# Kernel tuning notes

Measured on AMD Instinct MI355X. Metric: run time of the kernel, lower is better.

Reference implementation:

```python
import jax, jax.numpy as jnp
import numpy as np
from jax.scipy.ndimage import map_coordinates

IMG = 256
N_ANG = 50
BATCH = 4
N_CNN = 32
IN_CH = 2


def _circle_mask(S):
    c = (S - 1) / 2.0
    yy, xx = jnp.meshgrid(jnp.arange(S, dtype=jnp.float32), jnp.arange(S, dtype=jnp.float32), indexing='ij')
    return (((yy - c) ** 2 + (xx - c) ** 2) <= (S / 2.0) ** 2).astype(jnp.float32)


def radon_forward(img, angles):
    # img [B,1,S,S] -> sinogram [B,1,A,S]; parallel-beam, clip_to_circle=True
    S = img.shape[-1]
    c = (S - 1) / 2.0
    img = img * _circle_mask(S)
    t = jnp.arange(S, dtype=jnp.float32) - c        # integration coord
    s = jnp.arange(S, dtype=jnp.float32) - c        # detector coord
    cos = jnp.cos(angles)[:, None, None]
    sin = jnp.sin(angles)[:, None, None]
    x = s[None, None, :] * cos - t[None, :, None] * sin   # [A,S,S]
    y = s[None, None, :] * sin + t[None, :, None] * cos
    coords = jnp.stack([y + c, x + c])                    # [2,A,S,S] (row, col)
    samp = jax.vmap(lambda im: map_coordinates(im, coords, order=1, mode='constant', cval=0.0))(img[:, 0])  # [B,A,S,S]
    return samp.sum(axis=2)[:, None]                      # sum over ray param -> [B,1,A,S]


def filter_sinogram(sino):
    # Ram-Lak FFT filter with zero-padding + FBP normalization
    S = sino.shape[-1]
    A = sino.shape[2]
    P = max(64, int(2 ** np.ceil(np.log2(2 * S))))
    f = jnp.fft.rfft(jnp.pad(sino, ((0, 0), (0, 0), (0, 0), (0, P - S))), axis=-1)
    ramp = 2.0 * jnp.fft.rfftfreq(P).astype(jnp.float32)
    out = jnp.fft.irfft(f * ramp, n=P, axis=-1)[..., :S]
    return out * (np.pi / (2.0 * A))


def radon_backprojection(sino, angles):
    # sino [B,1,A,S] -> image [B,1,S,S]
    B, _, A, S = sino.shape
    c = (S - 1) / 2.0
    yy, xx = jnp.meshgrid(jnp.arange(S, dtype=jnp.float32) - c, jnp.arange(S, dtype=jnp.float32) - c, indexing='ij')
    cos = jnp.cos(angles)[:, None, None]
    sin = jnp.sin(angles)[:, None, None]
    det = xx[None] * cos + yy[None] * sin + c             # [A,S,S] detector coord
    sino2 = sino[:, 0]                                    # [B,A,S]

    def interp_one(sino_a, idx):
        # sino_a [B,S], idx [S,S] -> [B,S,S] linear interp, zero outside
        i0 = jnp.clip(jnp.floor(idx).astype(jnp.int32), 0, S - 2)
        w = idx - i0
        v = sino_a[:, i0] * (1.0 - w) + sino_a[:, i0 + 1] * w
        valid = (idx >= 0.0) & (idx <= S - 1.0)
        return jnp.where(valid, v, 0.0)

    bp = jax.vmap(interp_one, in_axes=(1, 0))(sino2, det).sum(axis=0)  # [B,S,S]
    return (bp * _circle_mask(S))[:, None]


def conv2d(x, w, b):
    y = jax.lax.conv_general_dilated(x, w, (1, 1), 'SAME', dimension_numbers=('NCHW', 'OIHW', 'NCHW'))
    return y + b[None, :, None, None]


def setup_inputs() -> dict:
    key = jax.random.key(0)
    ks = jax.random.split(key, 10)
    angles = jnp.asarray(np.linspace(0, np.pi, N_ANG, endpoint=False), dtype=jnp.float32)
    return {
        'x_sinogram': jax.random.normal(ks[0], (BATCH, 1, N_ANG, IMG), dtype=jnp.float32),
        'y_img_prev': jax.random.normal(ks[1], (BATCH, 1, IMG, IMG), dtype=jnp.float32),
        'y_img_concat_prev': jax.random.normal(ks[2], (BATCH, 1, IMG, IMG), dtype=jnp.float32),
        'angles': angles,
        'step': jnp.float32(1.0),
        'w1': jax.random.normal(ks[3], (N_CNN, IN_CH, 3, 3), dtype=jnp.float32) * 0.1,
        'b1': jnp.zeros((N_CNN,), dtype=jnp.float32),
        'w2': jax.random.normal(ks[4], (N_CNN, N_CNN, 3, 3), dtype=jnp.float32) * 0.1,
        'b2': jnp.zeros((N_CNN,), dtype=jnp.float32),
        'w3': jax.random.normal(ks[5], (1, N_CNN, 3, 3), dtype=jnp.float32) * 0.1,
        'b3': jnp.zeros((1,), dtype=jnp.float32),
    }


def reference(x_sinogram, y_img_prev, y_img_concat_prev, angles, step, w1, b1, w2, b2, w3, b3):
    Ay = radon_forward(y_img_prev, angles)                 # [B,1,A,S]
    diff = Ay - x_sinogram
    filt = filter_sinogram(diff)
    fbp = radon_backprojection(filt, angles)               # [B,1,S,S]
    y_img_update = y_img_prev + step * fbp
    y_cat = jnp.concatenate([y_img_update, y_img_concat_prev], axis=1)  # [B,2,S,S]
    h = jax.nn.relu(conv2d(y_cat, w1, b1))
    h = jax.nn.relu(conv2d(h, w2, b2))
    y_img = conv2d(h, w3, b3)
    return (y_img, y_img_update)
```

## Files before the change

### kernel.cpp

```cpp
#include <hip/hip_runtime.h>
#include <math.h>

#define IMGS 256
#define NANG 50
#define BATCH 4
#define NCNN 32
#define PIX (IMGS*IMGS)
#define NPIX (BATCH*PIX)

#define PROW 258
#define PPIX (PROW*PROW)
#define PB   (PPIX*NCNN)

#define OFF_FILT  0
#define OFF_W2BF  51200
#define OFF_H1P   55808

static constexpr double PI_D = 3.14159265358979323846;

typedef unsigned short u16;
typedef unsigned int   u32;
typedef unsigned long long u64;
typedef __bf16 bfrag __attribute__((ext_vector_type(8)));
typedef float  ffrag __attribute__((ext_vector_type(4)));

__device__ __forceinline__ u16 f2bf(float f) {
    u32 u = __float_as_uint(f);
    u += 0x7fffu + ((u >> 16) & 1u);
    return (u16)(u >> 16);
}

#define RPITCH_D 131
__global__ __launch_bounds__(1024, 4) void k_A(const float* __restrict__ angles,
                                               const float* __restrict__ yprev,
                                               const float* __restrict__ xsino,
                                               const float* __restrict__ w2,
                                               float* __restrict__ ws) {
    __shared__ u16 limg[258 * 262];
    __shared__ float spart[1024];
    __shared__ float staps[512];
    __shared__ float srow[256];
    int tid = threadIdx.x;
    int gid = blockIdx.x;
    if (gid >= 200) {
        int i = (gid - 200) * 1024 + tid;
        if (i < 9216) {
            int t = i >> 10, oc = (i >> 5) & 31, ic = i & 31;
            ((u16*)(ws + OFF_W2BF))[i] = f2bf(w2[(oc * 32 + ic) * 9 + t]);
        }
        return;
    }
    u32* l32 = (u32*)limg;
    int ra = gid;
    int a = ra % NANG, b = ra / NANG;

    if (tid < 511) {
        int d = tid - 255;
        int n = d < 0 ? -d : d;
        double g;
        if (n == 0) {
            g = 0.5;
        } else {
            double th = PI_D * (double)n / 256.0;
            double S = (256.0 * cos(255.0 * th) - 255.0 * cos(256.0 * th) - 1.0)
                       / (2.0 * (1.0 - cos(th)));
            double sign = (n & 1) ? -1.0 : 1.0;
            g = (sign + S / 128.0) / 512.0;
        }
        staps[tid] = (float)(g * PI_D / 100.0);
    }

    for (int z = tid; z < 772; z += 1024) {
        int addr;
        if (z < 258)      addr = z * RPITCH_D;
        else if (z < 516) addr = (z - 258) * RPITCH_D + 129;
        else if (z < 644) addr = (z - 516) + 1;
        else              addr = 257 * RPITCH_D + (z - 644) + 1;
        l32[addr] = 0;
    }
    const float* __restrict__ src = yprev + b * PIX;
    for (int idx = tid; idx < 16384; idx += 1024) {
        int r = idx >> 6, c4 = (idx & 63) << 2;
        float4 v = *(const float4*)(src + r * 256 + c4);
        float di = (float)r - 127.5f;
        float rr = di * di;
        float d0 = (float)c4 - 127.5f;
        v.x = (rr + d0 * d0 <= 16384.0f) ? v.x : 0.0f;
        v.y = (rr + (d0 + 1.0f) * (d0 + 1.0f) <= 16384.0f) ? v.y : 0.0f;
        v.z = (rr + (d0 + 2.0f) * (d0 + 2.0f) <= 16384.0f) ? v.z : 0.0f;
        v.w = (rr + (d0 + 3.0f) * (d0 + 3.0f) <= 16384.0f) ? v.w : 0.0f;
        u32 p0 = (u32)f2bf(v.x) | ((u32)f2bf(v.y) << 16);
        u32 p1 = (u32)f2bf(v.z) | ((u32)f2bf(v.w) << 16);
        int dw = (r + 1) * RPITCH_D + (c4 >> 1) + 1;
        l32[dw] = p0; l32[dw + 1] = p1;
    }
    __syncthreads();

    float a_ = angles[a];
    float cs = cosf(a_), sn = sinf(a_);
    int lane = tid & 63, w = tid >> 6;
    int s8 = lane & 7, t8 = lane >> 3;
    int sA = w * 16 + s8;
    float scA = (float)sA - 127.5f;

    float loA = (float)(w * 16) - 127.5f, hiA = loA + 7.0f;
    float loB = loA + 8.0f,               hiB = hiA + 8.0f;
    float s2minA = fminf(loA * loA, hiA * hiA);
    float s2maxA = fmaxf(loA * loA, hiA * hiA);
    float s2minB = fminf(loB * loB, hiB * hiB);
    float s2maxB = fmaxf(loB * loB, hiB * hiB);
    float s2min  = fminf(s2minA, s2minB);
    float s2max  = fmaxf(s2maxA, s2maxB);
    float hmax = sqrtf(16770.25f - s2min);
    int j_lo = max(0, (int)ceilf((120.5f - hmax) * 0.125f));
    int j_hi = min(31, (int)floorf((127.5f + hmax) * 0.125f));

    float tc0 = (float)t8 - 127.5f + 8.0f * (float)j_lo;
    float rowA = scA * sn + tc0 * cs + 127.5f;
    float colA = scA * cs - tc0 * sn + 127.5f;
    float rowB = rowA + 8.0f * sn;
    float colB = colA + 8.0f * cs;
    float cs8 = 8.0f * cs, sn8 = 8.0f * sn;
    float accA = 0.0f, accB = 0.0f;
    #pragma unroll 2
    for (int j = j_lo; j <= j_hi; ++j) {
        float t0j = 8.0f * (float)j - 127.5f;
        float t7j = t0j + 7.0f;
        float tmax2 = fmaxf(t0j * t0j, t7j * t7j);
        if (s2max + tmax2 <= 16384.0f) {
            #pragma unroll
            for (int hh = 0; hh < 2; ++hh) {
                float rowv = hh ? rowB : rowA;
                float colv = hh ? colB : colA;
                float fr = floorf(rowv), fc = floorf(colv);
                float wr = rowv - fr, wc = colv - fc;
                int i0 = (int)fr, j0 = (int)fc;
                int ca = j0 + 2;
                int ka = ca >> 1;
                int sh = (ca & 1) << 4;
                int dw = (i0 + 1) * RPITCH_D + ka;
                u32 A = l32[dw],            C = l32[dw + 1];
                u32 B = l32[dw + RPITCH_D], D = l32[dw + RPITCH_D + 1];
                u32 top = (u32)((((u64)C << 32) | (u64)A) >> sh);
                u32 bot = (u32)((((u64)D << 32) | (u64)B) >> sh);
                float tl = __uint_as_float(top << 16);
                float tr_ = __uint_as_float(top & 0xffff0000u);
                float bl = __uint_as_float(bot << 16);
                float br = __uint_as_float(bot & 0xffff0000u);
                float tv = tl + (tr_ - tl) * wc;
                float bv = bl + (br - bl) * wc;
                float sv = tv + (bv - tv) * wr;
                if (hh) accB += sv; else accA += sv;
            }
        } else {
            #pragma unroll
            for (int hh = 0; hh < 2; ++hh) {
                float rowv = hh ? rowB : rowA;
                float colv = hh ? colB : colA;
                float fr = floorf(rowv), fc = floorf(colv);
                float wr = rowv - fr, wc = colv - fc;
                int i0 = (int)fr, j0 = (int)fc;
                bool valid = (rowv > -1.0f) & (rowv < 256.0f) & (colv > -1.0f) & (colv < 256.0f);
                int i0c = min(max(i0, -1), 255);
                int j0c = min(max(j0, -1), 255);
                int ca = j0c + 2;
                int ka = ca >> 1;
                int sh = (ca & 1) << 4;
                int dw = (i0c + 1) * RPITCH_D + ka;
                u32 A = l32[dw],            C = l32[dw + 1];
                u32 B = l32[dw + RPITCH_D], D = l32[dw + RPITCH_D + 1];
                u32 top = (u32)((((u64)C << 32) | (u64)A) >> sh);
                u32 bot = (u32)((((u64)D << 32) | (u64)B) >> sh);
                float tl = __uint_as_float(top << 16);
                float tr_ = __uint_as_float(top & 0xffff0000u);
                float bl = __uint_as_float(bot << 16);
                float br = __uint_as_float(bot & 0xffff0000u);
                float tv = tl + (tr_ - tl) * wc;
                float bv = bl + (br - bl) * wc;
                float sv = tv + (bv - tv) * wr;
                sv = valid ? sv : 0.0f;
                if (hh) accB += sv; else accA += sv;
            }
        }
        rowA += cs8; colA -= sn8; rowB += cs8; colB -= sn8;
    }
    accA += __shfl_xor(accA, 8, 64);
    accA += __shfl_xor(accA, 16, 64);
    accA += __shfl_xor(accA, 32, 64);
    accB += __shfl_xor(accB, 8, 64);
    accB += __shfl_xor(accB, 16, 64);
    accB += __shfl_xor(accB, 32, 64);
    if (t8 == 0) { spart[sA] = accA; spart[sA + 8] = accB; }
    __syncthreads();
    if (tid < 256)
        srow[tid] = spart[tid] - xsino[ra * 256 + tid];
    __syncthreads();
    {
        int s = tid & 255, q = tid >> 8;
        float fa = 0.0f;
        int m0 = q * 64;
        #pragma unroll 8
        for (int m = m0; m < m0 + 64; ++m) fa += srow[m] * staps[s - m + 255];
        spart[tid] = fa;
    }
    __syncthreads();
    if (tid < 256)
        ws[OFF_FILT + ra * 256 + tid] =
            spart[tid] + spart[tid + 256] + spart[tid + 512] + spart[tid + 768];
}

__global__ __launch_bounds__(512, 4) void k_B(const float* __restrict__ angles,
                                              const float* __restrict__ yprev,
                                              const float* __restrict__ yconc,
                                              const float* __restrict__ stepp,
                                              const float* __restrict__ w1,
                                              const float* __restrict__ b1,
                                              float* __restrict__ ws,
                                              float* __restrict__ dout) {
    __shared__ float sf[NANG * 256];
    __shared__ __align__(16) float supd[4][260];
    __shared__ __align__(16) float sy2[4][260];
    __shared__ float scs[NANG], ssn[NANG];
    int tid = threadIdx.x;
    int b = blockIdx.x >> 7, tile = blockIdx.x & 127;
    int y0 = tile << 1;

    {
        const float4* s4 = (const float4*)(ws + OFF_FILT + b * (NANG * 256));
        float4* d4 = (float4*)sf;
        for (int idx = tid; idx < NANG * 64; idx += 512) d4[idx] = s4[idx];
    }
    if (tid < NANG) {
        float a_ = angles[tid];
        scs[tid] = cosf(a_); ssn[tid] = sinf(a_);
    }
    if (tid < 8) supd[tid >> 1][(tid & 1) * 257] = 0.0f;
    for (int idx = tid; idx < 4 * 258; idx += 512) {
        int r = idx / 258, x = idx % 258;
        int iy = y0 - 1 + r, ix = x - 1;
        sy2[r][x] = ((unsigned)iy < 256u && (unsigned)ix < 256u)
                        ? yconc[b * PIX + iy * 256 + ix] : 0.0f;
    }
    if (tid < 144) {
        int px_i = tile * 9 + (tid >> 4), dw = tid & 15;
        if (px_i < 1028) {
            int y, x;
            if (px_i < 516) { y = (px_i < 258) ? 0 : 257; x = px_i % 258; }
            else            { int j = px_i - 516; y = 1 + (j >> 1); x = (j & 1) * 257; }
            u32* p = (u32*)((u16*)(ws + OFF_H1P) + b * PB + (y * PROW + x) * NCNN);
            p[dw] = 0;
        }
    }
    __syncthreads();

    float step = stepp[0];
    {
        int j = tid & 255, r0 = tid >> 8;
        float xx = (float)j - 127.5f;
        float yy0 = (float)(y0 - 1 + r0) - 127.5f;
        float acc[2] = {0.0f, 0.0f};
        #pragma unroll 5
        for (int a = 0; a < NANG; ++a) {
            float cs = scs[a], sn = ssn[a];
            float f0 = xx * cs + yy0 * sn + 127.5f;
            float idxf[2] = {f0, f0 + sn + sn};
            #pragma unroll
            for (int k = 0; k < 2; ++k) {
                float fl = floorf(idxf[k]);
                int i0 = (int)fl;
                i0 = min(max(i0, 0), 254);
                float w = idxf[k] - (float)i0;
                float v = sf[a * 256 + i0] * (1.0f - w) + sf[a * 256 + i0 + 1] * w;
                acc[k] += (idxf[k] >= 0.0f && idxf[k] <= 255.0f) ? v : 0.0f;
            }
        }
        #pragma unroll
        for (int k = 0; k < 2; ++k) {
            int r = r0 + 2 * k;
            int iy = y0 - 1 + r;
            float val = 0.0f;
            if ((unsigned)iy < 256u) {
                float yy = (float)iy - 127.5f;
                float m = (xx * xx + yy * yy <= 16384.0f) ? 1.0f : 0.0f;
                val = yprev[b * PIX + iy * 256 + j] + step * acc[k] * m;
                if (r >= 1 && r <= 2)
                    dout[NPIX + b * PIX + iy * 256 + j] = val;
            }
            supd[r][j + 1] = val;
        }
    }
    __syncthreads();

    {
        int wave = tid >> 6, lane = tid & 63;
        int oc0 = wave * 4;
        float W[72];
        const float4* wsrc = (const float4*)(w1 + oc0 * 18);
        #pragma unroll
        for (int i = 0; i < 18; ++i) ((float4*)W)[i] = wsrc[i];
        float bb0 = b1[oc0], bb1 = b1[oc0 + 1], bb2 = b1[oc0 + 2], bb3 = b1[oc0 + 3];
        u16* h1base = (u16*)(ws + OFF_H1P) + b * PB;
        #pragma unroll
        for (int it = 0; it < 4; ++it) {
            int px0 = it * 128 + lane * 2;
            int rr = px0 >> 8, x0 = px0 & 255;
            int oy = y0 + rr;
            float a00 = bb0, a01 = bb1, a02 = bb2, a03 = bb3;
            float a10 = bb0, a11 = bb1, a12 = bb2, a13 = bb3;
            #pragma unroll
            for (int ky = 0; ky < 3; ++ky) {
                float2 ua = *(const float2*)&supd[rr + ky][x0];
                float2 ub = *(const float2*)&supd[rr + ky][x0 + 2];
                float2 ca = *(const float2*)&sy2[rr + ky][x0];
                float2 cb = *(const float2*)&sy2[rr + ky][x0 + 2];
                float u[4]  = {ua.x, ua.y, ub.x, ub.y};
                float c6[4] = {ca.x, ca.y, cb.x, cb.y};
                #pragma unroll
                for (int kx = 0; kx < 3; ++kx) {
                    int t = ky * 3 + kx;
                    float u0 = u[kx],     c0 = c6[kx];
                    float u1 = u[kx + 1], c1 = c6[kx + 1];
                    a00 += u0 * W[t]      + c0 * W[9 + t];
                    a01 += u0 * W[18 + t] + c0 * W[27 + t];
                    a02 += u0 * W[36 + t] + c0 * W[45 + t];
                    a03 += u0 * W[54 + t] + c0 * W[63 + t];
                    a10 += u1 * W[t]      + c1 * W[9 + t];
                    a11 += u1 * W[18 + t] + c1 * W[27 + t];
                    a12 += u1 * W[36 + t] + c1 * W[45 + t];
                    a13 += u1 * W[54 + t] + c1 * W[63 + t];
                }
            }
            u32 q00 = (u32)f2bf(fmaxf(a00, 0.0f)) | ((u32)f2bf(fmaxf(a01, 0.0f)) << 16);
            u32 q01 = (u32)f2bf(fmaxf(a02, 0.0f)) | ((u32)f2bf(fmaxf(a03, 0.0f)) << 16);
            u32 q10 = (u32)f2bf(fmaxf(a10, 0.0f)) | ((u32)f2bf(fmaxf(a11, 0.0f)) << 16);
            u32 q11 = (u32)f2bf(fmaxf(a12, 0.0f)) | ((u32)f2bf(fmaxf(a13, 0.0f)) << 16);
            u32* op0 = (u32*)(h1base + ((oy + 1) * PROW + (x0 + 1)) * NCNN + oc0);
            u32* op1 = (u32*)(h1base + ((oy + 1) * PROW + (x0 + 2)) * NCNN + oc0);
            op0[0] = q00; op0[1] = q01;
            op1[0] = q10; op1[1] = q11;
        }
    }
}

#define H2PITCH 36
__global__ __launch_bounds__(512, 4) void k_C(const float* __restrict__ b2,
                                              const float* __restrict__ w3,
                                              const float* __restrict__ b3,
                                              float* __restrict__ ws,
                                              float* __restrict__ dout) {
    __shared__ __align__(16) u16 sh2[4 * 258 * H2PITCH];
    __shared__ __align__(8) u32 swp[9 * 16];
    u32* l32 = (u32*)sh2;
    int tid = threadIdx.x;
    int b = blockIdx.x >> 7, tile = blockIdx.x & 127;
    int y0 = tile << 1;

    if (tid < 144) {
        int t = tid >> 4, kd = tid & 15;
        swp[tid] = (u32)f2bf(w3[(2 * kd) * 9 + t]) | ((u32)f2bf(w3[(2 * kd + 1) * 9 + t]) << 16);
    }
    if (tid < 144) {
        int r = tid / 36, rem = tid % 36;
        int col = (rem < 18) ? 0 : 257, dw = rem % 18;
        l32[(r * 258 + col) * 18 + dw] = 0;
    }
    #pragma unroll
    for (int r = 0; r < 4; ++r) {
        int hy = y0 - 1 + r;
        if (hy < 0 || hy > 255)
            for (int idx = tid; idx < 258 * 18; idx += 512)
                l32[r * 258 * 18 + idx] = 0;
    }
    __syncthreads();

    const u16* __restrict__ w2bf = (const u16*)(ws + OFF_W2BF);
    const u16* __restrict__ h1b  = (const u16*)(ws + OFF_H1P) + b * PB;
    int wave = tid >> 6, lane = tid & 63;
    int m = lane & 15, quad = lane >> 4;
    bfrag Bf[9][2];
    #pragma unroll
    for (int t = 0; t < 9; ++t) {
        const u16* wp = w2bf + t * 1024 + m * 32 + quad * 8;
        Bf[t][0] = *(const bfrag*)(wp);
        Bf[t][1] = *(const bfrag*)(wp + 16 * 32);
    }
    float bias0 = b2[m], bias1 = b2[m + 16];
    #pragma unroll
    for (int k = 0; k < 8; ++k) {
        int tl = wave + (k << 3);
        int ridx = tl >> 4, xt = tl & 15;
        int hy = y0 - 1 + ridx;
        bool valid = (unsigned)hy < 256u;
        int hyc = min(max(hy, 0), 255);
        int xs = xt << 4;
        bfrag A0[3], A1[3];
        #pragma unroll
        for (int tx = 0; tx < 3; ++tx)
            A0[tx] = *(const bfrag*)(h1b + ((hyc + 0) * PROW + xs + m + tx) * NCNN + quad * 8);
        #pragma unroll
        for (int tx = 0; tx < 3; ++tx)
            A1[tx] = *(const bfrag*)(h1b + ((hyc + 1) * PROW + xs + m + tx) * NCNN + quad * 8);
        ffrag c0 = {0.f, 0.f, 0.f, 0.f}, c1 = {0.f, 0.f, 0.f, 0.f};
        #pragma unroll
        for (int tx = 0; tx < 3; ++tx) {
            c0 = __builtin_amdgcn_mfma_f32_16x16x32_bf16(A0[tx], Bf[tx][0], c0, 0, 0, 0);
            c1 = __builtin_amdgcn_mfma_f32_16x16x32_bf16(A0[tx], Bf[tx][1], c1, 0, 0, 0);
        }
        #pragma unroll
        for (int tx = 0; tx < 3; ++tx)
            A0[tx] = *(const bfrag*)(h1b + ((hyc + 2) * PROW + xs + m + tx) * NCNN + quad * 8);
        #pragma unroll
        for (int tx = 0; tx < 3; ++tx) {
            c0 = __builtin_amdgcn_mfma_f32_16x16x32_bf16(A1[tx], Bf[3 + tx][0], c0, 0, 0, 0);
            c1 = __builtin_amdgcn_mfma_f32_16x16x32_bf16(A1[tx], Bf[3 + tx][1], c1, 0, 0, 0);
        }
        #pragma unroll
        for (int tx = 0; tx < 3; ++tx) {
            c0 = __builtin_amdgcn_mfma_f32_16x16x32_bf16(A0[tx], Bf[6 + tx][0], c0, 0, 0, 0);
            c1 = __builtin_amdgcn_mfma_f32_16x16x32_bf16(A0[tx], Bf[6 + tx][1], c1, 0, 0, 0);
        }
        if (valid) {
            #pragma unroll
            for (int r = 0; r < 4; ++r) {
                int px = xs + quad * 4 + r;
                u16* op = sh2 + (ridx * 258 + px + 1) * H2PITCH;
                op[m]      = f2bf(fmaxf(c0[r] + bias0, 0.0f));
                op[m + 16] = f2bf(fmaxf(c1[r] + bias1, 0.0f));
            }
        }
    }
    __syncthreads();

    {
        int rr = tid >> 8, x = tid & 255;
        int oy = y0 + rr;
        float acc = b3[0];
        #pragma unroll
        for (int ky = 0; ky < 3; ++ky) {
            #pragma unroll
            for (int cx = 0; cx < 3; ++cx) {
                int t = ky * 3 + cx;
                const uint2* q2 = (const uint2*)(l32 + ((rr + ky) * 258 + x + cx) * 18);
                const uint2* w2p = (const uint2*)(swp + t * 16);
                #pragma unroll
                for (int kd = 0; kd < 8; ++kd) {
                    uint2 hv = q2[kd];
                    uint2 wv = w2p[kd];
                    acc += __uint_as_float(hv.x << 16) * __uint_as_float(wv.x << 16)
                         + __uint_as_float(hv.x & 0xffff0000u) * __uint_as_float(wv.x & 0xffff0000u)
                         + __uint_as_float(hv.y << 16) * __uint_as_float(wv.y << 16)
                         + __uint_as_float(hv.y & 0xffff0000u) * __uint_as_float(wv.y & 0xffff0000u);
                }
            }
        }
        dout[b * PIX + oy * 256 + x] = acc;
    }
}

extern "C" void kernel_launch(void* const* d_in, const int* in_sizes, int n_in,
                              void* d_out, int out_size, void* d_ws, size_t ws_size,
                              hipStream_t stream) {
    const float* xsino  = (const float*)d_in[0];
    const float* yprev  = (const float*)d_in[1];
    const float* yconc  = (const float*)d_in[2];
    const float* angles = (const float*)d_in[3];
    const float* stepp  = (const float*)d_in[4];
    const float* w1 = (const float*)d_in[5];
    const float* b1 = (const float*)d_in[6];
    const float* w2 = (const float*)d_in[7];
    const float* b2 = (const float*)d_in[8];
    const float* w3 = (const float*)d_in[9];
    const float* b3 = (const float*)d_in[10];
    float* out = (float*)d_out;
    float* ws  = (float*)d_ws;

    k_A<<<209, 1024, 0, stream>>>(angles, yprev, xsino, w2, ws);
    k_B<<<BATCH * 128, 512, 0, stream>>>(angles, yprev, yconc, stepp, w1, b1, ws, out);
    k_C<<<BATCH * 128, 512, 0, stream>>>(b2, w3, b3, ws, out);
}
```

Before: 172.4 us.

## Store conv1 output in channel-planar layout and read filtered sinogram from global

Changes the intermediate h1 buffer from pixel-interleaved 32-channel layout to 8 planes of 4 channels each, so each wave in k_B writes contiguous 8-byte chunks per pixel. k_C reassembles MFMA A-fragments from two planes with two 8-byte loads each. k_B also drops its 51 KB shared-memory copy of the filtered sinogram and gathers directly from global/L1, and raises the launch-bounds occupancy hint from 4 to 6. The risks are more scattered global gathers in the backprojection and split, narrower loads in k_C.

Measured after the change: 233.7 us. 35.5% more time.

```diff
diff --git a/kernel.cpp b/kernel.cpp
--- a/kernel.cpp
+++ b/kernel.cpp
@@ -209,7 +209,7 @@
             spart[tid] + spart[tid + 256] + spart[tid + 512] + spart[tid + 768];
 }
 
-__global__ __launch_bounds__(512, 4) void k_B(const float* __restrict__ angles,
+__global__ __launch_bounds__(512, 6) void k_B(const float* __restrict__ angles,
                                               const float* __restrict__ yprev,
                                               const float* __restrict__ yconc,
                                               const float* __restrict__ stepp,
@@ -217,19 +217,14 @@
                                               const float* __restrict__ b1,
                                               float* __restrict__ ws,
                                               float* __restrict__ dout) {
-    __shared__ float sf[NANG * 256];
     __shared__ __align__(16) float supd[4][260];
     __shared__ __align__(16) float sy2[4][260];
     __shared__ float scs[NANG], ssn[NANG];
     int tid = threadIdx.x;
     int b = blockIdx.x >> 7, tile = blockIdx.x & 127;
     int y0 = tile << 1;
-
-    {
-        const float4* s4 = (const float4*)(ws + OFF_FILT + b * (NANG * 256));
-        float4* d4 = (float4*)sf;
-        for (int idx = tid; idx < NANG * 64; idx += 512) d4[idx] = s4[idx];
-    }
+    const float* __restrict__ sfg = ws + OFF_FILT + b * (NANG * 256);
+
     if (tid < NANG) {
         float a_ = angles[tid];
         scs[tid] = cosf(a_); ssn[tid] = sinf(a_);
@@ -242,12 +237,13 @@
                         ? yconc[b * PIX + iy * 256 + ix] : 0.0f;
     }
     if (tid < 144) {
-        int px_i = tile * 9 + (tid >> 4), dw = tid & 15;
+        int px_i = tile * 9 + (tid >> 4);
         if (px_i < 1028) {
             int y, x;
             if (px_i < 516) { y = (px_i < 258) ? 0 : 257; x = px_i % 258; }
             else            { int j = px_i - 516; y = 1 + (j >> 1); x = (j & 1) * 257; }
-            u32* p = (u32*)((u16*)(ws + OFF_H1P) + b * PB + (y * PROW + x) * NCNN);
+            int plane = (tid >> 1) & 7, dw = tid & 1;
+            u32* p = (u32*)((u16*)(ws + OFF_H1P) + b * PB + (plane * PPIX + y * PROW + x) * 4);
             p[dw] = 0;
         }
     }
@@ -270,7 +266,7 @@
                 int i0 = (int)fl;
                 i0 = min(max(i0, 0), 254);
                 float w = idxf[k] - (float)i0;
-                float v = sf[a * 256 + i0] * (1.0f - w) + sf[a * 256 + i0 + 1] * w;
+                float v = sfg[a * 256 + i0] * (1.0f - w) + sfg[a * 256 + i0 + 1] * w;
                 acc[k] += (idxf[k] >= 0.0f && idxf[k] <= 255.0f) ? v : 0.0f;
             }
         }
@@ -299,7 +295,7 @@
         #pragma unroll
         for (int i = 0; i < 18; ++i) ((float4*)W)[i] = wsrc[i];
         float bb0 = b1[oc0], bb1 = b1[oc0 + 1], bb2 = b1[oc0 + 2], bb3 = b1[oc0 + 3];
-        u16* h1base = (u16*)(ws + OFF_H1P) + b * PB;
+        u16* pl = (u16*)(ws + OFF_H1P) + b * PB + wave * (PPIX * 4);
         #pragma unroll
         for (int it = 0; it < 4; ++it) {
             int px0 = it * 128 + lane * 2;
@@ -334,15 +330,24 @@
             u32 q01 = (u32)f2bf(fmaxf(a02, 0.0f)) | ((u32)f2bf(fmaxf(a03, 0.0f)) << 16);
             u32 q10 = (u32)f2bf(fmaxf(a10, 0.0f)) | ((u32)f2bf(fmaxf(a11, 0.0f)) << 16);
             u32 q11 = (u32)f2bf(fmaxf(a12, 0.0f)) | ((u32)f2bf(fmaxf(a13, 0.0f)) << 16);
-            u32* op0 = (u32*)(h1base + ((oy + 1) * PROW + (x0 + 1)) * NCNN + oc0);
-            u32* op1 = (u32*)(h1base + ((oy + 1) * PROW + (x0 + 2)) * NCNN + oc0);
-            op0[0] = q00; op0[1] = q01;
-            op1[0] = q10; op1[1] = q11;
+            u32* op = (u32*)(pl + ((oy + 1) * PROW + (x0 + 1)) * 4);
+            *(uint2*)(op)     = make_uint2(q00, q01);
+            *(uint2*)(op + 2) = make_uint2(q10, q11);
         }
     }
 }
 
 #define H2PITCH 36
+__device__ __forceinline__ bfrag ld_frag(const u16* __restrict__ h1b, int q,
+                                         int row, int col) {
+    const u16* base = h1b + (row * PROW + col) * 4;
+    uint2 lo = *(const uint2*)(base + (2 * q)     * (PPIX * 4));
+    uint2 hi = *(const uint2*)(base + (2 * q + 1) * (PPIX * 4));
+    bfrag A;
+    ((uint2*)&A)[0] = lo;
+    ((uint2*)&A)[1] = hi;
+    return A;
+}
 __global__ __launch_bounds__(512, 4) void k_C(const float* __restrict__ b2,
                                               const float* __restrict__ w3,
                                               const float* __restrict__ b3,
@@ -396,10 +401,10 @@
         bfrag A0[3], A1[3];
         #pragma unroll
         for (int tx = 0; tx < 3; ++tx)
-            A0[tx] = *(const bfrag*)(h1b + ((hyc + 0) * PROW + xs + m + tx) * NCNN + quad * 8);
+            A0[tx] = ld_frag(h1b, quad, hyc + 0, xs + m + tx);
         #pragma unroll
         for (int tx = 0; tx < 3; ++tx)
-            A1[tx] = *(const bfrag*)(h1b + ((hyc + 1) * PROW + xs + m + tx) * NCNN + quad * 8);
+            A1[tx] = ld_frag(h1b, quad, hyc + 1, xs + m + tx);
         ffrag c0 = {0.f, 0.f, 0.f, 0.f}, c1 = {0.f, 0.f, 0.f, 0.f};
         #pragma unroll
         for (int tx = 0; tx < 3; ++tx) {
@@ -408,7 +413,7 @@
         }
         #pragma unroll
         for (int tx = 0; tx < 3; ++tx)
-            A0[tx] = *(const bfrag*)(h1b + ((hyc + 2) * PROW + xs + m + tx) * NCNN + quad * 8);
+            A0[tx] = ld_frag(h1b, quad, hyc + 2, xs + m + tx);
         #pragma unroll
         for (int tx = 0; tx < 3; ++tx) {
             c0 = __builtin_amdgcn_mfma_f32_16x16x32_bf16(A1[tx], Bf[3 + tx][0], c0, 0, 0, 0);
```

## Fuse backprojection, conv1 and conv2/conv3 into one kernel with LDS-resident h1

Applied to the files above, without the earlier changes.

Merges k_B and k_C into a single kernel that recomputes an 8-row halo of the updated image per tile, runs conv1 into shared memory in two column halves, then runs the MFMA conv2 and conv3 straight from LDS. This removes the global round trip of the 32-channel bf16 h1 tensor and one kernel launch. In exchange it recomputes backprojection and conv1 on halo rows (8 rows computed for 2 output rows), needs about 143KB of LDS (occupancy hint cut to 2 blocks), and adds extra barriers between the halves.

New measurement: 175.8 us. About the same (+1.9%).

```diff
diff --git a/kernel.cpp b/kernel.cpp
--- a/kernel.cpp
+++ b/kernel.cpp
@@ -8,13 +8,8 @@
 #define PIX (IMGS*IMGS)
 #define NPIX (BATCH*PIX)
 
-#define PROW 258
-#define PPIX (PROW*PROW)
-#define PB   (PPIX*NCNN)
-
 #define OFF_FILT  0
 #define OFF_W2BF  51200
-#define OFF_H1P   55808
 
 static constexpr double PI_D = 3.14159265358979323846;
 
@@ -209,18 +204,40 @@
             spart[tid] + spart[tid + 256] + spart[tid + 512] + spart[tid + 768];
 }
 
-__global__ __launch_bounds__(512, 4) void k_B(const float* __restrict__ angles,
-                                              const float* __restrict__ yprev,
-                                              const float* __restrict__ yconc,
-                                              const float* __restrict__ stepp,
-                                              const float* __restrict__ w1,
-                                              const float* __restrict__ b1,
-                                              float* __restrict__ ws,
-                                              float* __restrict__ dout) {
-    __shared__ float sf[NANG * 256];
-    __shared__ __align__(16) float supd[4][260];
-    __shared__ __align__(16) float sy2[4][260];
-    __shared__ float scs[NANG], ssn[NANG];
+#define H2PITCH 36
+#define SM_SF    0
+#define SM_H1    0
+#define SM_H2    51200
+#define SM_SUPD  125504
+#define SM_SY2   133824
+#define SM_SCS   142144
+#define SM_SSN   142344
+#define SM_SWP   142544
+#define SM_TOTAL 143120
+#define H1QSTRIDE (6*130*8)
+
+__global__ __launch_bounds__(512, 2) void k_BC(const float* __restrict__ angles,
+                                               const float* __restrict__ yprev,
+                                               const float* __restrict__ yconc,
+                                               const float* __restrict__ stepp,
+                                               const float* __restrict__ w1,
+                                               const float* __restrict__ b1,
+                                               const float* __restrict__ b2,
+                                               const float* __restrict__ w3,
+                                               const float* __restrict__ b3,
+                                               float* __restrict__ ws,
+                                               float* __restrict__ dout) {
+    __shared__ __align__(16) unsigned char smem[SM_TOTAL];
+    float* sf   = (float*)(smem + SM_SF);
+    u16*   h1q  = (u16*)(smem + SM_H1);
+    u16*   sh2  = (u16*)(smem + SM_H2);
+    u32*   l32c = (u32*)(smem + SM_H2);
+    float (*supd)[260] = (float(*)[260])(smem + SM_SUPD);
+    float (*sy2)[260]  = (float(*)[260])(smem + SM_SY2);
+    float* scs = (float*)(smem + SM_SCS);
+    float* ssn = (float*)(smem + SM_SSN);
+    u32*   swp = (u32*)(smem + SM_SWP);
+
     int tid = threadIdx.x;
     int b = blockIdx.x >> 7, tile = blockIdx.x & 127;
     int y0 = tile << 1;
@@ -234,148 +251,76 @@
         float a_ = angles[tid];
         scs[tid] = cosf(a_); ssn[tid] = sinf(a_);
     }
-    if (tid < 8) supd[tid >> 1][(tid & 1) * 257] = 0.0f;
-    for (int idx = tid; idx < 4 * 258; idx += 512) {
-        int r = idx / 258, x = idx % 258;
-        int iy = y0 - 1 + r, ix = x - 1;
-        sy2[r][x] = ((unsigned)iy < 256u && (unsigned)ix < 256u)
+    if (tid < 144) {
+        int t = tid >> 4, kd = tid & 15;
+        swp[tid] = (u32)f2bf(w3[(2 * kd) * 9 + t]) | ((u32)f2bf(w3[(2 * kd + 1) * 9 + t]) << 16);
+    }
+    if (tid < 32) {
+        int r = tid >> 2, c4 = tid & 3;
+        supd[r][(c4 < 2) ? c4 : (c4 + 256)] = 0.0f;
+    }
+    for (int idx = tid; idx < 8 * 260; idx += 512) {
+        int r = idx / 260, c = idx - r * 260;
+        int iy = y0 - 3 + r, ix = c - 2;
+        sy2[r][c] = ((unsigned)iy < 256u && (unsigned)ix < 256u)
                         ? yconc[b * PIX + iy * 256 + ix] : 0.0f;
     }
-    if (tid < 144) {
-        int px_i = tile * 9 + (tid >> 4), dw = tid & 15;
-        if (px_i < 1028) {
-            int y, x;
-            if (px_i < 516) { y = (px_i < 258) ? 0 : 257; x = px_i % 258; }
-            else            { int j = px_i - 516; y = 1 + (j >> 1); x = (j & 1) * 257; }
-            u32* p = (u32*)((u16*)(ws + OFF_H1P) + b * PB + (y * PROW + x) * NCNN);
-            p[dw] = 0;
-        }
-    }
-    __syncthreads();
-
-    float step = stepp[0];
+    __syncthreads();
+
     {
         int j = tid & 255, r0 = tid >> 8;
         float xx = (float)j - 127.5f;
-        float yy0 = (float)(y0 - 1 + r0) - 127.5f;
-        float acc[2] = {0.0f, 0.0f};
-        #pragma unroll 5
+        float yyb = (float)(y0 - 3 + r0) - 127.5f;
+        float ac0 = 0.f, ac1 = 0.f, ac2 = 0.f, ac3 = 0.f;
+        #pragma unroll 2
         for (int a = 0; a < NANG; ++a) {
             float cs = scs[a], sn = ssn[a];
-            float f0 = xx * cs + yy0 * sn + 127.5f;
-            float idxf[2] = {f0, f0 + sn + sn};
-            #pragma unroll
-            for (int k = 0; k < 2; ++k) {
-                float fl = floorf(idxf[k]);
-                int i0 = (int)fl;
-                i0 = min(max(i0, 0), 254);
-                float w = idxf[k] - (float)i0;
-                float v = sf[a * 256 + i0] * (1.0f - w) + sf[a * 256 + i0 + 1] * w;
-                acc[k] += (idxf[k] >= 0.0f && idxf[k] <= 255.0f) ? v : 0.0f;
-            }
-        }
+            float d2 = sn + sn;
+            float f0 = xx * cs + yyb * sn + 127.5f;
+            float f1 = f0 + d2, f2 = f1 + d2, f3 = f2 + d2;
+            #define BPSAMP(ff, accv) { \
+                float fl = floorf(ff); int i0 = (int)fl; \
+                i0 = min(max(i0, 0), 254); \
+                float wq = ff - (float)i0; \
+                float v = sf[a * 256 + i0] * (1.0f - wq) + sf[a * 256 + i0 + 1] * wq; \
+                accv += (ff >= 0.0f && ff <= 255.0f) ? v : 0.0f; }
+            BPSAMP(f0, ac0) BPSAMP(f1, ac1) BPSAMP(f2, ac2) BPSAMP(f3, ac3)
+            #undef BPSAMP
+        }
+        float step = stepp[0];
+        float accs[4] = {ac0, ac1, ac2, ac3};
         #pragma unroll
-        for (int k = 0; k < 2; ++k) {
-            int r = r0 + 2 * k;
-            int iy = y0 - 1 + r;
+        for (int k = 0; k < 4; ++k) {
+            int lr = r0 + 2 * k;
+            int iy = y0 - 3 + lr;
             float val = 0.0f;
             if ((unsigned)iy < 256u) {
                 float yy = (float)iy - 127.5f;
-                float m = (xx * xx + yy * yy <= 16384.0f) ? 1.0f : 0.0f;
-                val = yprev[b * PIX + iy * 256 + j] + step * acc[k] * m;
-                if (r >= 1 && r <= 2)
+                float mk = (xx * xx + yy * yy <= 16384.0f) ? 1.0f : 0.0f;
+                val = yprev[b * PIX + iy * 256 + j] + step * accs[k] * mk;
+                if (iy >= y0 && iy <= y0 + 1)
                     dout[NPIX + b * PIX + iy * 256 + j] = val;
             }
-            supd[r][j + 1] = val;
-        }
-    }
-    __syncthreads();
-
-    {
-        int wave = tid >> 6, lane = tid & 63;
-        int oc0 = wave * 4;
-        float W[72];
-        const float4* wsrc = (const float4*)(w1 + oc0 * 18);
-        #pragma unroll
-        for (int i = 0; i < 18; ++i) ((float4*)W)[i] = wsrc[i];
-        float bb0 = b1[oc0], bb1 = b1[oc0 + 1], bb2 = b1[oc0 + 2], bb3 = b1[oc0 + 3];
-        u16* h1base = (u16*)(ws + OFF_H1P) + b * PB;
-        #pragma unroll
-        for (int it = 0; it < 4; ++it) {
-            int px0 = it * 128 + lane * 2;
-            int rr = px0 >> 8, x0 = px0 & 255;
-            int oy = y0 + rr;
-            float a00 = bb0, a01 = bb1, a02 = bb2, a03 = bb3;
-            float a10 = bb0, a11 = bb1, a12 = bb2, a13 = bb3;
-            #pragma unroll
-            for (int ky = 0; ky < 3; ++ky) {
-                float2 ua = *(const float2*)&supd[rr + ky][x0];
-                float2 ub = *(const float2*)&supd[rr + ky][x0 + 2];
-                float2 ca = *(const float2*)&sy2[rr + ky][x0];
-                float2 cb = *(const float2*)&sy2[rr + ky][x0 + 2];
-                float u[4]  = {ua.x, ua.y, ub.x, ub.y};
-                float c6[4] = {ca.x, ca.y, cb.x, cb.y};
-                #pragma unroll
-                for (int kx = 0; kx < 3; ++kx) {
-                    int t = ky * 3 + kx;
-                    float u0 = u[kx],     c0 = c6[kx];
-                    float u1 = u[kx + 1], c1 = c6[kx + 1];
-                    a00 += u0 * W[t]      + c0 * W[9 + t];
-                    a01 += u0 * W[18 + t] + c0 * W[27 + t];
-                    a02 += u0 * W[36 + t] + c0 * W[45 + t];
-                    a03 += u0 * W[54 + t] + c0 * W[63 + t];
-                    a10 += u1 * W[t]      + c1 * W[9 + t];
-                    a11 += u1 * W[18 + t] + c1 * W[27 + t];
-                    a12 += u1 * W[36 + t] + c1 * W[45 + t];
-                    a13 += u1 * W[54 + t] + c1 * W[63 + t];
-                }
-            }
-            u32 q00 = (u32)f2bf(fmaxf(a00, 0.0f)) | ((u32)f2bf(fmaxf(a01, 0.0f)) << 16);
-            u32 q01 = (u32)f2bf(fmaxf(a02, 0.0f)) | ((u32)f2bf(fmaxf(a03, 0.0f)) << 16);
-            u32 q10 = (u32)f2bf(fmaxf(a10, 0.0f)) | ((u32)f2bf(fmaxf(a11, 0.0f)) << 16);
-            u32 q11 = (u32)f2bf(fmaxf(a12, 0.0f)) | ((u32)f2bf(fmaxf(a13, 0.0f)) << 16);
-            u32* op0 = (u32*)(h1base + ((oy + 1) * PROW + (x0 + 1)) * NCNN + oc0);
-            u32* op1 = (u32*)(h1base + ((oy + 1) * PROW + (x0 + 2)) * NCNN + oc0);
-            op0[0] = q00; op0[1] = q01;
-            op1[0] = q10; op1[1] = q11;
-        }
-    }
-}
-
-#define H2PITCH 36
-__global__ __launch_bounds__(512, 4) void k_C(const float* __restrict__ b2,
-                                              const float* __restrict__ w3,
-                                              const float* __restrict__ b3,
-                                              float* __restrict__ ws,
-                                              float* __restrict__ dout) {
-    __shared__ __align__(16) u16 sh2[4 * 258 * H2PITCH];
-    __shared__ __align__(8) u32 swp[9 * 16];
-    u32* l32 = (u32*)sh2;
-    int tid = threadIdx.x;
-    int b = blockIdx.x >> 7, tile = blockIdx.x & 127;
-    int y0 = tile << 1;
-
-    if (tid < 144) {
-        int t = tid >> 4, kd = tid & 15;
-        swp[tid] = (u32)f2bf(w3[(2 * kd) * 9 + t]) | ((u32)f2bf(w3[(2 * kd + 1) * 9 + t]) << 16);
-    }
+            supd[lr][j + 2] = val;
+        }
+    }
+    __syncthreads();
+
     if (tid < 144) {
         int r = tid / 36, rem = tid % 36;
         int col = (rem < 18) ? 0 : 257, dw = rem % 18;
-        l32[(r * 258 + col) * 18 + dw] = 0;
+        l32c[(r * 258 + col) * 18 + dw] = 0;
     }
     #pragma unroll
     for (int r = 0; r < 4; ++r) {
         int hy = y0 - 1 + r;
         if (hy < 0 || hy > 255)
             for (int idx = tid; idx < 258 * 18; idx += 512)
-                l32[r * 258 * 18 + idx] = 0;
-    }
-    __syncthreads();
+                l32c[r * 258 * 18 + idx] = 0;
+    }
 
     const u16* __restrict__ w2bf = (const u16*)(ws + OFF_W2BF);
-    const u16* __restrict__ h1b  = (const u16*)(ws + OFF_H1P) + b * PB;
-    int wave = tid >> 6, lane = tid & 63;
+    int wv = tid >> 6, lane = tid & 63;
     int m = lane & 15, quad = lane >> 4;
     bfrag Bf[9][2];
     #pragma unroll
@@ -385,51 +330,119 @@
         Bf[t][1] = *(const bfrag*)(wp + 16 * 32);
     }
     float bias0 = b2[m], bias1 = b2[m + 16];
-    #pragma unroll
-    for (int k = 0; k < 8; ++k) {
-        int tl = wave + (k << 3);
-        int ridx = tl >> 4, xt = tl & 15;
-        int hy = y0 - 1 + ridx;
-        bool valid = (unsigned)hy < 256u;
-        int hyc = min(max(hy, 0), 255);
-        int xs = xt << 4;
-        bfrag A0[3], A1[3];
-        #pragma unroll
-        for (int tx = 0; tx < 3; ++tx)
-            A0[tx] = *(const bfrag*)(h1b + ((hyc + 0) * PROW + xs + m + tx) * NCNN + quad * 8);
-        #pragma unroll
-        for (int tx = 0; tx < 3; ++tx)
-            A1[tx] = *(const bfrag*)(h1b + ((hyc + 1) * PROW + xs + m + tx) * NCNN + quad * 8);
-        ffrag c0 = {0.f, 0.f, 0.f, 0.f}, c1 = {0.f, 0.f, 0.f, 0.f};
-        #pragma unroll
-        for (int tx = 0; tx < 3; ++tx) {
-            c0 = __builtin_amdgcn_mfma_f32_16x16x32_bf16(A0[tx], Bf[tx][0], c0, 0, 0, 0);
-            c1 = __builtin_amdgcn_mfma_f32_16x16x32_bf16(A0[tx], Bf[tx][1], c1, 0, 0, 0);
-        }
-        #pragma unroll
-        for (int tx = 0; tx < 3; ++tx)
-            A0[tx] = *(const bfrag*)(h1b + ((hyc + 2) * PROW + xs + m + tx) * NCNN + quad * 8);
-        #pragma unroll
-        for (int tx = 0; tx < 3; ++tx) {
-            c0 = __builtin_amdgcn_mfma_f32_16x16x32_bf16(A1[tx], Bf[3 + tx][0], c0, 0, 0, 0);
-            c1 = __builtin_amdgcn_mfma_f32_16x16x32_bf16(A1[tx], Bf[3 + tx][1], c1, 0, 0, 0);
-        }
-        #pragma unroll
-        for (int tx = 0; tx < 3; ++tx) {
-            c0 = __builtin_amdgcn_mfma_f32_16x16x32_bf16(A0[tx], Bf[6 + tx][0], c0, 0, 0, 0);
-            c1 = __builtin_amdgcn_mfma_f32_16x16x32_bf16(A0[tx], Bf[6 + tx][1], c1, 0, 0, 0);
-        }
-        if (valid) {
+
+    for (int xh = 0; xh < 2; ++xh) {
+        {
+            int oc0 = wv * 4, qq = wv >> 1, hh = wv & 1;
+            float W[72];
+            const float4* wsrc = (const float4*)(w1 + oc0 * 18);
             #pragma unroll
-            for (int r = 0; r < 4; ++r) {
-                int px = xs + quad * 4 + r;
-                u16* op = sh2 + (ridx * 258 + px + 1) * H2PITCH;
-                op[m]      = f2bf(fmaxf(c0[r] + bias0, 0.0f));
-                op[m + 16] = f2bf(fmaxf(c1[r] + bias1, 0.0f));
-            }
-        }
-    }
-    __syncthreads();
+            for (int i = 0; i < 18; ++i) ((float4*)W)[i] = wsrc[i];
+            float bb0 = b1[oc0], bb1 = b1[oc0 + 1], bb2 = b1[oc0 + 2], bb3 = b1[oc0 + 3];
+            u16* hq = h1q + qq * H1QSTRIDE + hh * 4;
+            for (int it = 0; it < 7; ++it) {
+                int idx = it * 64 + lane;
+                if (idx < 390) {
+                    int lr = idx / 65, pp = idx - lr * 65;
+                    int ir = y0 - 2 + lr;
+                    int P = xh * 128 + 2 * pp - 1;
+                    int cb = P + 1 + 2 - xh * 256;
+                    int cgb = P + 1;
+                    float a00 = bb0, a01 = bb1, a02 = bb2, a03 = bb3;
+                    float a10 = bb0, a11 = bb1, a12 = bb2, a13 = bb3;
+                    #pragma unroll
+                    for (int ky = 0; ky < 3; ++ky) {
+                        float2 ua = *(const float2*)&supd[lr + ky][cgb];
+                        float2 ub = *(const float2*)&supd[lr + ky][cgb + 2];
+                        float2 ca = *(const float2*)&sy2[lr + ky][cgb];
+                        float2 cb2 = *(const float2*)&sy2[lr + ky][cgb + 2];
+                        float u[4]  = {ua.x, ua.y, ub.x, ub.y};
+                        float c6[4] = {ca.x, ca.y, cb2.x, cb2.y};
+                        #pragma unroll
+                        for (int kx = 0; kx < 3; ++kx) {
+                            int t = ky * 3 + kx;
+                            float u0 = u[kx],     c0 = c6[kx];
+                            float u1 = u[kx + 1], c1 = c6[kx + 1];
+                            a00 += u0 * W[t]      + c0 * W[9 + t];
+                            a01 += u0 * W[18 + t] + c0 * W[27 + t];
+                            a02 += u0 * W[36 + t] + c0 * W[45 + t];
+                            a03 += u0 * W[54 + t] + c0 * W[63 + t];
+                            a10 += u1 * W[t]      + c1 * W[9 + t];
+                            a11 += u1 * W[18 + t] + c1 * W[27 + t];
+                            a12 += u1 * W[36 + t] + c1 * W[45 + t];
+                            a13 += u1 * W[54 + t] + c1 * W[63 + t];
+                        }
+                    }
+                    bool rowOK = (unsigned)ir < 256u;
+                    bool v0 = rowOK && ((unsigned)P < 256u);
+                    bool v1 = rowOK && ((unsigned)(P + 1) < 256u);
+                    u32 q00 = 0, q01 = 0, q10 = 0, q11 = 0;
+                    if (v0) {
+                        q00 = (u32)f2bf(fmaxf(a00, 0.f)) | ((u32)f2bf(fmaxf(a01, 0.f)) << 16);
+                        q01 = (u32)f2bf(fmaxf(a02, 0.f)) | ((u32)f2bf(fmaxf(a03, 0.f)) << 16);
+                    }
+                    if (v1) {
+                        q10 = (u32)f2bf(fmaxf(a10, 0.f)) | ((u32)f2bf(fmaxf(a11, 0.f)) << 16);
+                        q11 = (u32)f2bf(fmaxf(a12, 0.f)) | ((u32)f2bf(fmaxf(a13, 0.f)) << 16);
+                    }
+                    int cl = 2 * pp;
+                    u32* op0 = (u32*)(hq + (lr * 130 + cl) * 8);
+                    u32* op1 = (u32*)(hq + (lr * 130 + cl + 1) * 8);
+                    op0[0] = q00; op0[1] = q01;
+                    op1[0] = q10; op1[1] = q11;
+                }
+            }
+        }
+        __syncthreads();
+
+        {
+            const u16* Abase = h1q + quad * H1QSTRIDE;
+            #pragma unroll
+            for (int k = 0; k < 4; ++k) {
+                int tl = wv + (k << 3);
+                int ridx = tl >> 3, xt8 = tl & 7;
+                int hy = y0 - 1 + ridx;
+                bool valid = (unsigned)hy < 256u;
+                int clb = (xt8 << 4) + m;
+                bfrag A0[3], A1[3];
+                #pragma unroll
+                for (int tx = 0; tx < 3; ++tx)
+                    A0[tx] = *(const bfrag*)(Abase + ((ridx + 0) * 130 + clb + tx) * 8);
+                #pragma unroll
+                for (int tx = 0; tx < 3; ++tx)
+                    A1[tx] = *(const bfrag*)(Abase + ((ridx + 1) * 130 + clb + tx) * 8);
+                ffrag c0 = {0.f, 0.f, 0.f, 0.f}, c1 = {0.f, 0.f, 0.f, 0.f};
+                #pragma unroll
+                for (int tx = 0; tx < 3; ++tx) {
+                    c0 = __builtin_amdgcn_mfma_f32_16x16x32_bf16(A0[tx], Bf[tx][0], c0, 0, 0, 0);
+                    c1 = __builtin_amdgcn_mfma_f32_16x16x32_bf16(A0[tx], Bf[tx][1], c1, 0, 0, 0);
+                }
+                #pragma unroll
+                for (int tx = 0; tx < 3; ++tx)
+                    A0[tx] = *(const bfrag*)(Abase + ((ridx + 2) * 130 + clb + tx) * 8);
+                #pragma unroll
+                for (int tx = 0; tx < 3; ++tx) {
+                    c0 = __builtin_amdgcn_mfma_f32_16x16x32_bf16(A1[tx], Bf[3 + tx][0], c0, 0, 0, 0);
+                    c1 = __builtin_amdgcn_mfma_f32_16x16x32_bf16(A1[tx], Bf[3 + tx][1], c1, 0, 0, 0);
+                }
+                #pragma unroll
+                for (int tx = 0; tx < 3; ++tx) {
+                    c0 = __builtin_amdgcn_mfma_f32_16x16x32_bf16(A0[tx], Bf[6 + tx][0], c0, 0, 0, 0);
+                    c1 = __builtin_amdgcn_mfma_f32_16x16x32_bf16(A0[tx], Bf[6 + tx][1], c1, 0, 0, 0);
+                }
+                if (valid) {
+                    #pragma unroll
+                    for (int r = 0; r < 4; ++r) {
+                        int px = xh * 128 + (xt8 << 4) + quad * 4 + r;
+                        u16* op = sh2 + (ridx * 258 + px + 1) * H2PITCH;
+                        op[m]      = f2bf(fmaxf(c0[r] + bias0, 0.0f));
+                        op[m + 16] = f2bf(fmaxf(c1[r] + bias1, 0.0f));
+                    }
+                }
+            }
+        }
+        __syncthreads();
+    }
 
     {
         int rr = tid >> 8, x = tid & 255;
@@ -440,16 +453,16 @@
             #pragma unroll
             for (int cx = 0; cx < 3; ++cx) {
                 int t = ky * 3 + cx;
-                const uint2* q2 = (const uint2*)(l32 + ((rr + ky) * 258 + x + cx) * 18);
+                const uint2* q2 = (const uint2*)(l32c + ((rr + ky) * 258 + x + cx) * 18);
                 const uint2* w2p = (const uint2*)(swp + t * 16);
                 #pragma unroll
                 for (int kd = 0; kd < 8; ++kd) {
                     uint2 hv = q2[kd];
-                    uint2 wv = w2p[kd];
-                    acc += __uint_as_float(hv.x << 16) * __uint_as_float(wv.x << 16)
-                         + __uint_as_float(hv.x & 0xffff0000u) * __uint_as_float(wv.x & 0xffff0000u)
-                         + __uint_as_float(hv.y << 16) * __uint_as_float(wv.y << 16)
-                         + __uint_as_float(hv.y & 0xffff0000u) * __uint_as_float(wv.y & 0xffff0000u);
+                    uint2 wvv = w2p[kd];
+                    acc += __uint_as_float(hv.x << 16) * __uint_as_float(wvv.x << 16)
+                         + __uint_as_float(hv.x & 0xffff0000u) * __uint_as_float(wvv.x & 0xffff0000u)
+                         + __uint_as_float(hv.y << 16) * __uint_as_float(wvv.y << 16)
+                         + __uint_as_float(hv.y & 0xffff0000u) * __uint_as_float(wvv.y & 0xffff0000u);
                 }
             }
         }
@@ -475,6 +488,6 @@
     float* ws  = (float*)d_ws;
 
     k_A<<<209, 1024, 0, stream>>>(angles, yprev, xsino, w2, ws);
-    k_B<<<BATCH * 128, 512, 0, stream>>>(angles, yprev, yconc, stepp, w1, b1, ws, out);
-    k_C<<<BATCH * 128, 512, 0, stream>>>(b2, w3, b3, ws, out);
+    k_BC<<<BATCH * 128, 512, 0, stream>>>(angles, yprev, yconc, stepp, w1, b1,
+                                          b2, w3, b3, ws, out);
 }
```
